# Kernel tuning notes

Measured on AMD Instinct MI355X. Metric: run time of the kernel, lower is better.

Reference implementation:

```python
import jax, jax.numpy as jnp
import numpy as np

N_CHO, N_JUNG, N_JONG = 19, 21, 28
N_COMPS = N_CHO + N_JUNG + N_JONG  # 68
N_STYLES = 32
B = 512
C, H, W = 128, 16, 16


def setup_inputs() -> dict:
    key = jax.random.key(0)
    ks = jax.random.split(key, 8)
    style_ids = jax.random.randint(ks[0], (B,), 0, N_STYLES, dtype=jnp.int64 if jax.config.jax_enable_x64 else jnp.int32)
    comp_ids = jax.random.randint(ks[1], (B, 3), 0, N_CHO, dtype=style_ids.dtype)  # valid for all 3 cols (19<=21,28)
    comp_feats = jax.random.normal(ks[2], (B, 3, C, H, W), dtype=jnp.float32)
    bias = jax.random.normal(ks[3], (N_COMPS, C, H, W), dtype=jnp.float32)
    fan = C * 9
    w1 = jax.random.normal(ks[4], (C, C, 3, 3), jnp.float32) / np.sqrt(fan)
    w2 = jax.random.normal(ks[5], (C, C, 3, 3), jnp.float32) / np.sqrt(fan)
    w3 = jax.random.normal(ks[6], (C, C, 3, 3), jnp.float32) / np.sqrt(fan)
    b1 = jnp.zeros((C,), jnp.float32)
    b2 = jnp.zeros((C,), jnp.float32)
    b3 = jnp.zeros((C,), jnp.float32)
    return {"style_ids": style_ids, "comp_ids": comp_ids, "comp_feats": comp_feats,
            "bias": bias, "w1": w1, "b1": b1, "w2": w2, "b2": b2, "w3": w3, "b3": b3}


def _conv_relu(x, w, b):
    # ConvBlock: 3x3 conv, pad 1, + ReLU (dmfont ConvBlock)
    y = jax.lax.conv_general_dilated(x, w, (1, 1), 'SAME',
                                     dimension_numbers=('NCHW', 'OIHW', 'NCHW'))
    return jax.nn.relu(y + b[None, :, None, None])


def reference(style_ids, comp_ids, comp_feats, bias, w1, b1, w2, b2, w3, b3):
    # comp_id_to_addr (kor): offset columns by [0, N_CHO, N_CHO+N_JUNG]
    offsets = jnp.array([0, N_CHO, N_CHO + N_JUNG], dtype=comp_ids.dtype)
    addrs = comp_ids + offsets[None, :]                       # [B, 3]
    keys = (style_ids[:, None] * N_COMPS + addrs).reshape(-1)  # [B*3]

    # DynamicMemory.write + read(reduction='mean') == scatter-mean by (style, addr) key
    feats = comp_feats.reshape(B * 3, C, H, W)
    nseg = N_STYLES * N_COMPS
    sums = jax.ops.segment_sum(feats, keys, num_segments=nseg)           # [nseg, C, H, W]
    cnts = jax.ops.segment_sum(jnp.ones((B * 3,), feats.dtype), keys, num_segments=nseg)
    means = sums / jnp.maximum(cnts, 1.0)[:, None, None, None]
    mem = means[keys].reshape(B, 3, C, H, W)

    # PersistentMemory: gather bias by addr, run 3-block conv hypernet, add
    pb = bias[addrs.reshape(-1)]                              # [B*3, C, H, W]
    pb = _conv_relu(pb, w1, b1)
    pb = _conv_relu(pb, w2, b2)
    pb = _conv_relu(pb, w3, b3)
    return mem + pb.reshape(B, 3, C, H, W)
```

## Files before the change

kernel.cpp:

```cpp
#include <hip/hip_runtime.h>

typedef __attribute__((ext_vector_type(8))) unsigned short ushort8_t;
typedef __attribute__((ext_vector_type(8))) __bf16 bf16x8;
typedef __attribute__((ext_vector_type(16))) float f32x16;

#define NSEG 2176
#define NITEM 1536

__device__ inline unsigned short f2bf(float f) {
    unsigned int b = __builtin_bit_cast(unsigned int, f);
    b += 0x7FFFu + ((b >> 16) & 1u);
    return (unsigned short)(b >> 16);
}
__device__ inline float bf2f(unsigned short h) {
    unsigned int b = ((unsigned int)h) << 16;
    return __builtin_bit_cast(float, b);
}

__global__ __launch_bounds__(256) void kA(const int* __restrict__ style,
                                          const int* __restrict__ cids,
                                          int* __restrict__ addr_g, int* __restrict__ key_g,
                                          int* __restrict__ rank_g, int* __restrict__ list_g,
                                          int* __restrict__ segstart_g, int* __restrict__ segcnt_g) {
    __shared__ int cnt[NSEG];
    __shared__ int sstart[NSEG];
    __shared__ int partial[256];
    const int tid = threadIdx.x;
    const int lane = tid & 63;
    const int wid = tid >> 6;
    for (int s = tid; s < NSEG; s += 256) cnt[s] = 0;
    __syncthreads();
    int myrank[6], mykey[6];
    #pragma unroll
    for (int k = 0; k < 6; ++k) {
        const int i = k * 256 + tid;
        const int b = i / 3, j = i - b * 3;
        const int off = (j == 0) ? 0 : (j == 1) ? 19 : 40;
        const int a = cids[i] + off;
        const int key = style[b] * 68 + a;
        addr_g[i] = a; key_g[i] = key;
        mykey[k] = key;
        myrank[k] = atomicAdd(&cnt[key], 1);
        rank_g[i] = myrank[k];
    }
    __syncthreads();
    const int base = tid * 9;
    int ssum = 0;
    for (int q = 0; q < 9; ++q) { int s = base + q; if (s < NSEG) ssum += cnt[s]; }
    partial[tid] = ssum;
    __syncthreads();
    if (wid == 0) {
        int s0 = partial[lane * 4 + 0], s1 = partial[lane * 4 + 1];
        int s2 = partial[lane * 4 + 2], s3 = partial[lane * 4 + 3];
        const int loc = s0 + s1 + s2 + s3;
        int pre = loc;
        #pragma unroll
        for (int d = 1; d < 64; d <<= 1) {
            const int o = __shfl_up(pre, d);
            if (lane >= d) pre += o;
        }
        pre -= loc;
        partial[lane * 4 + 0] = pre;
        partial[lane * 4 + 1] = pre + s0;
        partial[lane * 4 + 2] = pre + s0 + s1;
        partial[lane * 4 + 3] = pre + s0 + s1 + s2;
    }
    __syncthreads();
    int run = partial[tid];
    for (int q = 0; q < 9; ++q) {
        int s = base + q;
        if (s < NSEG) { sstart[s] = run; segstart_g[s] = run; segcnt_g[s] = cnt[s]; run += cnt[s]; }
    }
    __syncthreads();
    #pragma unroll
    for (int k = 0; k < 6; ++k) {
        const int i = k * 256 + tid;
        list_g[sstart[mykey[k]] + myrank[k]] = i;
    }
}

__global__ __launch_bounds__(256) void kW(const float* __restrict__ w1,
                                          const float* __restrict__ w2,
                                          const float* __restrict__ w3,
                                          unsigned short* __restrict__ Bp) {
    const int t = blockIdx.x * 256 + threadIdx.x;
    if (t >= 3 * 147456) return;
    const int l = t / 147456;
    const int o = t - l * 147456;
    const int slot = o & 7;
    const int co = (o >> 3) & 127;
    const int kb = o >> 10;
    const int tap = kb >> 4;
    const int ci = ((kb & 15) << 3) | slot;
    const float* w = (l == 0) ? w1 : (l == 1) ? w2 : w3;
    Bp[t] = f2bf(w[(co * 128 + ci) * 9 + tap]);
}

__global__ __launch_bounds__(512) void kConvF(const float* __restrict__ bias_in,
                                              const unsigned short* __restrict__ Bp,
                                              const float* __restrict__ b1,
                                              const float* __restrict__ b2,
                                              const float* __restrict__ b3,
                                              unsigned short* __restrict__ pbu_out) {
    __shared__ char lds[65536];
    const int tid = threadIdx.x;
    const int u = blockIdx.x;

    {
        const float* src = bias_in + (size_t)u * 32768;
        const int m = tid & 255;
        const int c0 = (tid >> 8) * 64;
        const int swz = (m & 15) << 4;
        #pragma unroll 4
        for (int c = c0; c < c0 + 64; ++c) {
            const float v = src[c * 256 + m];
            const int off = (m * 256 + c * 2) ^ swz;
            *(unsigned short*)(lds + off) = f2bf(v);
        }
    }
    __syncthreads();

    const int lane = tid & 63;
    const int wid = tid >> 6;
    const int wm = wid >> 1;
    const int wn = wid & 1;
    const int lrow = lane & 31;
    const int lhi = lane >> 5;

    for (int layer = 0; layer < 3; ++layer) {
        const unsigned short* Bpl = Bp + (size_t)layer * 147456;
        const float* bv = (layer == 0) ? b1 : (layer == 1) ? b2 : b3;

        f32x16 acc[2][2] = {};

        #pragma unroll 2
        for (int kk = 0; kk < 72; ++kk) {
            const int tap = kk >> 3;
            const int t3 = tap / 3;
            const int oh = t3 - 1;
            const int ow = (tap - t3 * 3) - 1;
            const int ci0 = (kk & 7) * 16 + lhi * 8;
            const int kb = kk * 2 + lhi;

            bf16x8 bfrag[2];
            #pragma unroll
            for (int t2 = 0; t2 < 2; ++t2) {
                const int co = (wn * 2 + t2) * 32 + lrow;
                bfrag[t2] = __builtin_bit_cast(bf16x8,
                    *(const ushort8_t*)(Bpl + ((size_t)(kb * 128 + co)) * 8));
            }
            bf16x8 afrag[2];
            #pragma unroll
            for (int t = 0; t < 2; ++t) {
                const int m = (wm * 2 + t) * 32 + lrow;
                const int h = (m >> 4) + oh;
                const int w = (m & 15) + ow;
                ushort8_t v = {0, 0, 0, 0, 0, 0, 0, 0};
                if ((unsigned)h < 16u && (unsigned)w < 16u) {
                    const int m2 = h * 16 + w;
                    const int off = (m2 * 256 + ci0 * 2) ^ ((m2 & 15) << 4);
                    v = *(const ushort8_t*)(lds + off);
                }
                afrag[t] = __builtin_bit_cast(bf16x8, v);
            }
            #pragma unroll
            for (int t = 0; t < 2; ++t)
                #pragma unroll
                for (int t2 = 0; t2 < 2; ++t2)
                    acc[t][t2] = __builtin_amdgcn_mfma_f32_32x32x16_bf16(
                        afrag[t], bfrag[t2], acc[t][t2], 0, 0, 0);
        }

        if (layer < 2) {
            unsigned short pk[2][2][16];
            #pragma unroll
            for (int t = 0; t < 2; ++t)
                #pragma unroll
                for (int t2 = 0; t2 < 2; ++t2) {
                    const int co = (wn * 2 + t2) * 32 + lrow;
                    const float bb = bv[co];
                    #pragma unroll
                    for (int r = 0; r < 16; ++r)
                        pk[t][t2][r] = f2bf(fmaxf(acc[t][t2][r] + bb, 0.0f));
                }
            __syncthreads();
            #pragma unroll
            for (int t = 0; t < 2; ++t)
                #pragma unroll
                for (int t2 = 0; t2 < 2; ++t2) {
                    const int co = (wn * 2 + t2) * 32 + lrow;
                    #pragma unroll
                    for (int r = 0; r < 16; ++r) {
                        const int m = (wm * 2 + t) * 32 + (r & 3) + 8 * (r >> 2) + 4 * lhi;
                        const int off = (m * 256 + co * 2) ^ ((m & 15) << 4);
                        *(unsigned short*)(lds + off) = pk[t][t2][r];
                    }
                }
            __syncthreads();
        } else {
            #pragma unroll
            for (int t2 = 0; t2 < 2; ++t2) {
                const int co = (wn * 2 + t2) * 32 + lrow;
                const float bb = bv[co];
                #pragma unroll
                for (int t = 0; t < 2; ++t) {
                    const int tmb = (wm * 2 + t) * 32;
                    #pragma unroll
                    for (int rq = 0; rq < 4; ++rq) {
                        const int m0 = tmb + 8 * rq + 4 * lhi;
                        ushort4 pkv;
                        pkv.x = f2bf(fmaxf(acc[t][t2][rq * 4 + 0] + bb, 0.0f));
                        pkv.y = f2bf(fmaxf(acc[t][t2][rq * 4 + 1] + bb, 0.0f));
                        pkv.z = f2bf(fmaxf(acc[t][t2][rq * 4 + 2] + bb, 0.0f));
                        pkv.w = f2bf(fmaxf(acc[t][t2][rq * 4 + 3] + bb, 0.0f));
                        *(ushort4*)(pbu_out + (size_t)u * 32768 + co * 256 + m0) = pkv;
                    }
                }
            }
        }
    }
}

__global__ __launch_bounds__(256) void kB(const float* __restrict__ feats,
                                          const unsigned short* __restrict__ pbu,
                                          const int* __restrict__ addr_g,
                                          const int* __restrict__ key_g,
                                          const int* __restrict__ rank_g,
                                          const int* __restrict__ list_g,
                                          const int* __restrict__ segstart_g,
                                          const int* __restrict__ segcnt_g,
                                          float* __restrict__ out) {
    const int i = blockIdx.y;
    if (rank_g[i] != 0) return;
    const int s = key_g[i];
    const int st = segstart_g[s];
    const int n = segcnt_g[s];
    const int e = blockIdx.x * 1024 + threadIdx.x * 4;
    float sx = 0.f, sy = 0.f, sz = 0.f, sw = 0.f;
    for (int t = 0; t < n; ++t) {
        const int j = list_g[st + t];
        const float4 v = *(const float4*)(feats + (size_t)j * 32768 + e);
        sx += v.x; sy += v.y; sz += v.z; sw += v.w;
    }
    const float inv = 1.0f / (float)n;
    sx *= inv; sy *= inv; sz *= inv; sw *= inv;
    for (int t = 0; t < n; ++t) {
        const int j = list_g[st + t];
        const int a = addr_g[j];
        const ushort4 p = *(const ushort4*)(pbu + (size_t)a * 32768 + e);
        float4 o;
        o.x = sx + bf2f(p.x);
        o.y = sy + bf2f(p.y);
        o.z = sz + bf2f(p.z);
        o.w = sw + bf2f(p.w);
        *(float4*)(out + (size_t)j * 32768 + e) = o;
    }
}

extern "C" void kernel_launch(void* const* d_in, const int* in_sizes, int n_in,
                              void* d_out, int out_size, void* d_ws, size_t ws_size,
                              hipStream_t stream) {
    const int* style   = (const int*)d_in[0];
    const int* cids    = (const int*)d_in[1];
    const float* feats = (const float*)d_in[2];
    const float* bias  = (const float*)d_in[3];
    const float* w1    = (const float*)d_in[4];
    const float* b1    = (const float*)d_in[5];
    const float* w2    = (const float*)d_in[6];
    const float* b2    = (const float*)d_in[7];
    const float* w3    = (const float*)d_in[8];
    const float* b3    = (const float*)d_in[9];
    float* out = (float*)d_out;
    char* ws = (char*)d_ws;

    int* addr_g     = (int*)(ws + 0);
    int* key_g      = (int*)(ws + 6144);
    int* rank_g     = (int*)(ws + 12288);
    int* list_g     = (int*)(ws + 18432);
    int* segstart_g = (int*)(ws + 24576);
    int* segcnt_g   = (int*)(ws + 33280);
    unsigned short* Bp  = (unsigned short*)(ws + 65536);
    unsigned short* pbu = (unsigned short*)(ws + 1048576);

    hipLaunchKernelGGL(kA, dim3(1), dim3(256), 0, stream,
                       style, cids, addr_g, key_g, rank_g, list_g, segstart_g, segcnt_g);
    hipLaunchKernelGGL(kW, dim3(1728), dim3(256), 0, stream, w1, w2, w3, Bp);
    hipLaunchKernelGGL(kConvF, dim3(68), dim3(512), 0, stream,
                       bias, Bp, b1, b2, b3, pbu);
    hipLaunchKernelGGL(kB, dim3(32, NITEM), dim3(256), 0, stream,
                       feats, pbu, addr_g, key_g, rank_g, list_g, segstart_g, segcnt_g, out);
}
```

Measured before the change: 431.1 us.

## Fuse index and weight-prep kernels, widen conv block, compact segment list for gather

Merges the weight-packing kernel and the segment-building kernel into one launch, with one extra block handling the index work. The conv kernel moves to 1024 threads with one M tile per wave and vectorized LDS staging of the bias input. The final gather kernel now iterates over a compacted list of non-empty segments, loads the persistent bias once per segment using the segment's address, and uses nontemporal loads and stores. This cuts launch overhead and early-exit blocks, in exchange for a larger conv block that may put more pressure on registers and occupancy.

```diff
diff --git a/kernel.cpp b/kernel.cpp
--- a/kernel.cpp
+++ b/kernel.cpp
@@ -3,6 +3,7 @@
 typedef __attribute__((ext_vector_type(8))) unsigned short ushort8_t;
 typedef __attribute__((ext_vector_type(8))) __bf16 bf16x8;
 typedef __attribute__((ext_vector_type(16))) float f32x16;
+typedef __attribute__((ext_vector_type(4))) float f32x4;
 
 #define NSEG 2176
 #define NITEM 1536
@@ -17,18 +18,37 @@
     return __builtin_bit_cast(float, b);
 }
 
-__global__ __launch_bounds__(256) void kA(const int* __restrict__ style,
-                                          const int* __restrict__ cids,
-                                          int* __restrict__ addr_g, int* __restrict__ key_g,
-                                          int* __restrict__ rank_g, int* __restrict__ list_g,
-                                          int* __restrict__ segstart_g, int* __restrict__ segcnt_g) {
+__global__ __launch_bounds__(256) void kAW(const int* __restrict__ style,
+                                           const int* __restrict__ cids,
+                                           const float* __restrict__ w1,
+                                           const float* __restrict__ w2,
+                                           const float* __restrict__ w3,
+                                           unsigned short* __restrict__ Bp,
+                                           int* __restrict__ list_g,
+                                           int* __restrict__ segstart_g, int* __restrict__ segcnt_g,
+                                           int* __restrict__ segkey_g, int* __restrict__ nseg_g) {
+    const int tid = threadIdx.x;
+    if (blockIdx.x < 1728) {
+        const int t = blockIdx.x * 256 + tid;
+        const int l = t / 147456;
+        const int o = t - l * 147456;
+        const int slot = o & 7;
+        const int co = (o >> 3) & 127;
+        const int kb = o >> 10;
+        const int tap = kb >> 4;
+        const int ci = ((kb & 15) << 3) | slot;
+        const float* w = (l == 0) ? w1 : (l == 1) ? w2 : w3;
+        Bp[t] = f2bf(w[(co * 128 + ci) * 9 + tap]);
+        return;
+    }
     __shared__ int cnt[NSEG];
     __shared__ int sstart[NSEG];
     __shared__ int partial[256];
-    const int tid = threadIdx.x;
+    __shared__ int nseg_sh;
     const int lane = tid & 63;
     const int wid = tid >> 6;
     for (int s = tid; s < NSEG; s += 256) cnt[s] = 0;
+    if (tid == 0) nseg_sh = 0;
     __syncthreads();
     int myrank[6], mykey[6];
     #pragma unroll
@@ -38,10 +58,8 @@
         const int off = (j == 0) ? 0 : (j == 1) ? 19 : 40;
         const int a = cids[i] + off;
         const int key = style[b] * 68 + a;
-        addr_g[i] = a; key_g[i] = key;
         mykey[k] = key;
         myrank[k] = atomicAdd(&cnt[key], 1);
-        rank_g[i] = myrank[k];
     }
     __syncthreads();
     const int base = tid * 9;
@@ -69,9 +87,14 @@
     int run = partial[tid];
     for (int q = 0; q < 9; ++q) {
         int s = base + q;
-        if (s < NSEG) { sstart[s] = run; segstart_g[s] = run; segcnt_g[s] = cnt[s]; run += cnt[s]; }
-    }
-    __syncthreads();
+        if (s < NSEG) {
+            sstart[s] = run; segstart_g[s] = run; segcnt_g[s] = cnt[s];
+            if (cnt[s] > 0) { const int ix = atomicAdd(&nseg_sh, 1); segkey_g[ix] = s; }
+            run += cnt[s];
+        }
+    }
+    __syncthreads();
+    if (tid == 0) nseg_g[0] = nseg_sh;
     #pragma unroll
     for (int k = 0; k < 6; ++k) {
         const int i = k * 256 + tid;
@@ -79,43 +102,30 @@
     }
 }
 
-__global__ __launch_bounds__(256) void kW(const float* __restrict__ w1,
-                                          const float* __restrict__ w2,
-                                          const float* __restrict__ w3,
-                                          unsigned short* __restrict__ Bp) {
-    const int t = blockIdx.x * 256 + threadIdx.x;
-    if (t >= 3 * 147456) return;
-    const int l = t / 147456;
-    const int o = t - l * 147456;
-    const int slot = o & 7;
-    const int co = (o >> 3) & 127;
-    const int kb = o >> 10;
-    const int tap = kb >> 4;
-    const int ci = ((kb & 15) << 3) | slot;
-    const float* w = (l == 0) ? w1 : (l == 1) ? w2 : w3;
-    Bp[t] = f2bf(w[(co * 128 + ci) * 9 + tap]);
-}
-
-__global__ __launch_bounds__(512) void kConvF(const float* __restrict__ bias_in,
-                                              const unsigned short* __restrict__ Bp,
-                                              const float* __restrict__ b1,
-                                              const float* __restrict__ b2,
-                                              const float* __restrict__ b3,
-                                              unsigned short* __restrict__ pbu_out) {
+__global__ __launch_bounds__(1024) void kConvF(const float* __restrict__ bias_in,
+                                               const unsigned short* __restrict__ Bp,
+                                               const float* __restrict__ b1,
+                                               const float* __restrict__ b2,
+                                               const float* __restrict__ b3,
+                                               unsigned short* __restrict__ pbu_out) {
     __shared__ char lds[65536];
     const int tid = threadIdx.x;
     const int u = blockIdx.x;
 
     {
         const float* src = bias_in + (size_t)u * 32768;
-        const int m = tid & 255;
-        const int c0 = (tid >> 8) * 64;
-        const int swz = (m & 15) << 4;
-        #pragma unroll 4
-        for (int c = c0; c < c0 + 64; ++c) {
-            const float v = src[c * 256 + m];
-            const int off = (m * 256 + c * 2) ^ swz;
-            *(unsigned short*)(lds + off) = f2bf(v);
+        const int c4 = tid & 31;
+        const int mbase = tid >> 5;
+        #pragma unroll
+        for (int it = 0; it < 8; ++it) {
+            const int m = mbase + 32 * it;
+            ushort4 pk;
+            pk.x = f2bf(src[(c4 * 4 + 0) * 256 + m]);
+            pk.y = f2bf(src[(c4 * 4 + 1) * 256 + m]);
+            pk.z = f2bf(src[(c4 * 4 + 2) * 256 + m]);
+            pk.w = f2bf(src[(c4 * 4 + 3) * 256 + m]);
+            const int off = (m * 256 + c4 * 8) ^ ((m & 15) << 4);
+            *(ushort4*)(lds + off) = pk;
         }
     }
     __syncthreads();
@@ -131,7 +141,7 @@
         const unsigned short* Bpl = Bp + (size_t)layer * 147456;
         const float* bv = (layer == 0) ? b1 : (layer == 1) ? b2 : b3;
 
-        f32x16 acc[2][2] = {};
+        f32x16 acc[2] = {};
 
         #pragma unroll 2
         for (int kk = 0; kk < 72; ++kk) {
@@ -149,53 +159,42 @@
                 bfrag[t2] = __builtin_bit_cast(bf16x8,
                     *(const ushort8_t*)(Bpl + ((size_t)(kb * 128 + co)) * 8));
             }
-            bf16x8 afrag[2];
-            #pragma unroll
-            for (int t = 0; t < 2; ++t) {
-                const int m = (wm * 2 + t) * 32 + lrow;
-                const int h = (m >> 4) + oh;
-                const int w = (m & 15) + ow;
-                ushort8_t v = {0, 0, 0, 0, 0, 0, 0, 0};
-                if ((unsigned)h < 16u && (unsigned)w < 16u) {
-                    const int m2 = h * 16 + w;
-                    const int off = (m2 * 256 + ci0 * 2) ^ ((m2 & 15) << 4);
-                    v = *(const ushort8_t*)(lds + off);
+            const int m = wm * 32 + lrow;
+            const int h = (m >> 4) + oh;
+            const int w = (m & 15) + ow;
+            ushort8_t v = {0, 0, 0, 0, 0, 0, 0, 0};
+            if ((unsigned)h < 16u && (unsigned)w < 16u) {
+                const int m2 = h * 16 + w;
+                const int off = (m2 * 256 + ci0 * 2) ^ ((m2 & 15) << 4);
+                v = *(const ushort8_t*)(lds + off);
+            }
+            const bf16x8 afrag = __builtin_bit_cast(bf16x8, v);
+            #pragma unroll
+            for (int t2 = 0; t2 < 2; ++t2)
+                acc[t2] = __builtin_amdgcn_mfma_f32_32x32x16_bf16(
+                    afrag, bfrag[t2], acc[t2], 0, 0, 0);
+        }
+
+        if (layer < 2) {
+            unsigned short pk[2][16];
+            #pragma unroll
+            for (int t2 = 0; t2 < 2; ++t2) {
+                const float bb = bv[(wn * 2 + t2) * 32 + lrow];
+                #pragma unroll
+                for (int r = 0; r < 16; ++r)
+                    pk[t2][r] = f2bf(fmaxf(acc[t2][r] + bb, 0.0f));
+            }
+            __syncthreads();
+            #pragma unroll
+            for (int t2 = 0; t2 < 2; ++t2) {
+                const int co = (wn * 2 + t2) * 32 + lrow;
+                #pragma unroll
+                for (int r = 0; r < 16; ++r) {
+                    const int m = wm * 32 + (r & 3) + 8 * (r >> 2) + 4 * lhi;
+                    const int off = (m * 256 + co * 2) ^ ((m & 15) << 4);
+                    *(unsigned short*)(lds + off) = pk[t2][r];
                 }
-                afrag[t] = __builtin_bit_cast(bf16x8, v);
-            }
-            #pragma unroll
-            for (int t = 0; t < 2; ++t)
-                #pragma unroll
-                for (int t2 = 0; t2 < 2; ++t2)
-                    acc[t][t2] = __builtin_amdgcn_mfma_f32_32x32x16_bf16(
-                        afrag[t], bfrag[t2], acc[t][t2], 0, 0, 0);
-        }
-
-        if (layer < 2) {
-            unsigned short pk[2][2][16];
-            #pragma unroll
-            for (int t = 0; t < 2; ++t)
-                #pragma unroll
-                for (int t2 = 0; t2 < 2; ++t2) {
-                    const int co = (wn * 2 + t2) * 32 + lrow;
-                    const float bb = bv[co];
-                    #pragma unroll
-                    for (int r = 0; r < 16; ++r)
-                        pk[t][t2][r] = f2bf(fmaxf(acc[t][t2][r] + bb, 0.0f));
-                }
-            __syncthreads();
-            #pragma unroll
-            for (int t = 0; t < 2; ++t)
-                #pragma unroll
-                for (int t2 = 0; t2 < 2; ++t2) {
-                    const int co = (wn * 2 + t2) * 32 + lrow;
-                    #pragma unroll
-                    for (int r = 0; r < 16; ++r) {
-                        const int m = (wm * 2 + t) * 32 + (r & 3) + 8 * (r >> 2) + 4 * lhi;
-                        const int off = (m * 256 + co * 2) ^ ((m & 15) << 4);
-                        *(unsigned short*)(lds + off) = pk[t][t2][r];
-                    }
-                }
+            }
             __syncthreads();
         } else {
             #pragma unroll
@@ -203,18 +202,14 @@
                 const int co = (wn * 2 + t2) * 32 + lrow;
                 const float bb = bv[co];
                 #pragma unroll
-                for (int t = 0; t < 2; ++t) {
-                    const int tmb = (wm * 2 + t) * 32;
-                    #pragma unroll
-                    for (int rq = 0; rq < 4; ++rq) {
-                        const int m0 = tmb + 8 * rq + 4 * lhi;
-                        ushort4 pkv;
-                        pkv.x = f2bf(fmaxf(acc[t][t2][rq * 4 + 0] + bb, 0.0f));
-                        pkv.y = f2bf(fmaxf(acc[t][t2][rq * 4 + 1] + bb, 0.0f));
-                        pkv.z = f2bf(fmaxf(acc[t][t2][rq * 4 + 2] + bb, 0.0f));
-                        pkv.w = f2bf(fmaxf(acc[t][t2][rq * 4 + 3] + bb, 0.0f));
-                        *(ushort4*)(pbu_out + (size_t)u * 32768 + co * 256 + m0) = pkv;
-                    }
+                for (int rq = 0; rq < 4; ++rq) {
+                    const int m0 = wm * 32 + 8 * rq + 4 * lhi;
+                    ushort4 pkv;
+                    pkv.x = f2bf(fmaxf(acc[t2][rq * 4 + 0] + bb, 0.0f));
+                    pkv.y = f2bf(fmaxf(acc[t2][rq * 4 + 1] + bb, 0.0f));
+                    pkv.z = f2bf(fmaxf(acc[t2][rq * 4 + 2] + bb, 0.0f));
+                    pkv.w = f2bf(fmaxf(acc[t2][rq * 4 + 3] + bb, 0.0f));
+                    *(ushort4*)(pbu_out + (size_t)u * 32768 + co * 256 + m0) = pkv;
                 }
             }
         }
@@ -223,37 +218,37 @@
 
 __global__ __launch_bounds__(256) void kB(const float* __restrict__ feats,
                                           const unsigned short* __restrict__ pbu,
-                                          const int* __restrict__ addr_g,
-                                          const int* __restrict__ key_g,
-                                          const int* __restrict__ rank_g,
                                           const int* __restrict__ list_g,
+                                          const int* __restrict__ segkey_g,
                                           const int* __restrict__ segstart_g,
                                           const int* __restrict__ segcnt_g,
+                                          const int* __restrict__ nseg_g,
                                           float* __restrict__ out) {
-    const int i = blockIdx.y;
-    if (rank_g[i] != 0) return;
-    const int s = key_g[i];
+    const int sy = blockIdx.y;
+    if (sy >= nseg_g[0]) return;
+    const int s = segkey_g[sy];
     const int st = segstart_g[s];
     const int n = segcnt_g[s];
+    const int a = s % 68;
     const int e = blockIdx.x * 1024 + threadIdx.x * 4;
-    float sx = 0.f, sy = 0.f, sz = 0.f, sw = 0.f;
+
+    f32x4 acc = {0.f, 0.f, 0.f, 0.f};
     for (int t = 0; t < n; ++t) {
         const int j = list_g[st + t];
-        const float4 v = *(const float4*)(feats + (size_t)j * 32768 + e);
-        sx += v.x; sy += v.y; sz += v.z; sw += v.w;
+        const f32x4 v = __builtin_nontemporal_load(
+            (const f32x4*)(feats + (size_t)j * 32768 + e));
+        acc += v;
     }
     const float inv = 1.0f / (float)n;
-    sx *= inv; sy *= inv; sz *= inv; sw *= inv;
+    const ushort4 p = *(const ushort4*)(pbu + (size_t)a * 32768 + e);
+    f32x4 o;
+    o.x = acc.x * inv + bf2f(p.x);
+    o.y = acc.y * inv + bf2f(p.y);
+    o.z = acc.z * inv + bf2f(p.z);
+    o.w = acc.w * inv + bf2f(p.w);
     for (int t = 0; t < n; ++t) {
         const int j = list_g[st + t];
-        const int a = addr_g[j];
-        const ushort4 p = *(const ushort4*)(pbu + (size_t)a * 32768 + e);
-        float4 o;
-        o.x = sx + bf2f(p.x);
-        o.y = sy + bf2f(p.y);
-        o.z = sz + bf2f(p.z);
-        o.w = sw + bf2f(p.w);
-        *(float4*)(out + (size_t)j * 32768 + e) = o;
+        __builtin_nontemporal_store(o, (f32x4*)(out + (size_t)j * 32768 + e));
     }
 }
 
@@ -273,20 +268,19 @@
     float* out = (float*)d_out;
     char* ws = (char*)d_ws;
 
-    int* addr_g     = (int*)(ws + 0);
-    int* key_g      = (int*)(ws + 6144);
-    int* rank_g     = (int*)(ws + 12288);
-    int* list_g     = (int*)(ws + 18432);
-    int* segstart_g = (int*)(ws + 24576);
-    int* segcnt_g   = (int*)(ws + 33280);
+    int* list_g     = (int*)(ws + 0);
+    int* segstart_g = (int*)(ws + 8192);
+    int* segcnt_g   = (int*)(ws + 16896);
+    int* segkey_g   = (int*)(ws + 25600);
+    int* nseg_g     = (int*)(ws + 34304);
     unsigned short* Bp  = (unsigned short*)(ws + 65536);
     unsigned short* pbu = (unsigned short*)(ws + 1048576);
 
-    hipLaunchKernelGGL(kA, dim3(1), dim3(256), 0, stream,
-                       style, cids, addr_g, key_g, rank_g, list_g, segstart_g, segcnt_g);
-    hipLaunchKernelGGL(kW, dim3(1728), dim3(256), 0, stream, w1, w2, w3, Bp);
-    hipLaunchKernelGGL(kConvF, dim3(68), dim3(512), 0, stream,
+    hipLaunchKernelGGL(kAW, dim3(1729), dim3(256), 0, stream,
+                       style, cids, w1, w2, w3, Bp,
+                       list_g, segstart_g, segcnt_g, segkey_g, nseg_g);
+    hipLaunchKernelGGL(kConvF, dim3(68), dim3(1024), 0, stream,
                        bias, Bp, b1, b2, b3, pbu);
     hipLaunchKernelGGL(kB, dim3(32, NITEM), dim3(256), 0, stream,
-                       feats, pbu, addr_g, key_g, rank_g, list_g, segstart_g, segcnt_g, out);
-}
+                       feats, pbu, list_g, segkey_g, segstart_g, segcnt_g, nseg_g, out);
+}
```

After: 431.4 us. Within noise of the previous version (+0.1%).
